# Performance work log

Measured on AMD Instinct MI355X. Metric: run time of the kernel, lower is better.

The kernel has to match this reference:

```python
import jax, jax.numpy as jnp
import numpy as np

COS_EPS = 1e-6
LN_EPS = 1e-5

def _cosine_sim(a, b):
    # PyTorch F.cosine_similarity(dim=1, eps): dot / (max(||a||,eps)*max(||b||,eps))
    dot = jnp.sum(a * b, axis=1)
    na = jnp.maximum(jnp.linalg.norm(a, axis=1), COS_EPS)
    nb = jnp.maximum(jnp.linalg.norm(b, axis=1), COS_EPS)
    return dot / (na * nb)

def _layer_norm(x, gamma, beta):
    mu = jnp.mean(x, axis=-1, keepdims=True)
    var = jnp.mean(jnp.square(x - mu), axis=-1, keepdims=True)
    return (x - mu) * jax.lax.rsqrt(var + LN_EPS) * gamma + beta

def setup_inputs() -> dict:
    B, I, H = 8192, 1024, 1024
    key = jax.random.key(0)
    ks = jax.random.split(key, 10)
    s_in = 1.0 / np.sqrt(I + H)
    s_im = 1.0 / np.sqrt(I)
    return {
        "x": jax.random.normal(ks[0], (B, I), jnp.float32),
        "hx": jax.random.normal(ks[1], (B, H), jnp.float32),
        "cx": jax.random.normal(ks[2], (B, H), jnp.float32),
        # main gate linear: [I+H, 4H]
        "W": jax.random.uniform(ks[3], (I + H, 4 * H), jnp.float32, -s_in, s_in),
        "b": jax.random.uniform(ks[4], (4 * H,), jnp.float32, -s_in, s_in),
        # input_mapped: [I, H]
        "Wm": jax.random.uniform(ks[5], (I, H), jnp.float32, -s_im, s_im),
        "bm": jax.random.uniform(ks[6], (H,), jnp.float32, -s_im, s_im),
        # 4 LayerNorms (i, f, g, o)
        "gammas": 1.0 + 0.1 * jax.random.normal(ks[7], (4, H), jnp.float32),
        "betas": 0.1 * jax.random.normal(ks[8], (4, H), jnp.float32),
    }

def reference(x, hx, cx, W, b, Wm, bm, gammas, betas):
    H = hx.shape[1]
    # cosine attention gate between mapped input and hidden state
    input_mapped = x @ Wm + bm                                   # [B, H]
    attn = jax.nn.sigmoid(_cosine_sim(input_mapped, hx))[:, None]  # [B, 1]
    x_mod = x + attn * x
    gates = jnp.concatenate([x_mod, hx], axis=1) @ W + b         # [B, 4H]
    i_g, f_g, g_g, o_g = jnp.split(gates, 4, axis=1)
    i_g = jax.nn.sigmoid(_layer_norm(i_g, gammas[0], betas[0]))
    f_g = jax.nn.sigmoid(_layer_norm(f_g, gammas[1], betas[1]))
    g_g = jnp.tanh(_layer_norm(g_g, gammas[2], betas[2]))
    o_g = jax.nn.sigmoid(_layer_norm(o_g, gammas[3], betas[3]))
    cx_new = f_g * cx + i_g * g_g
    hx_new = o_g * jnp.tanh(cx_new)
    gate_co = jax.nn.sigmoid((_cosine_sim(hx_new, cx_new)[:, None] + 1.0) / 2.0)
    hx_modulated = hx_new + hx_new * gate_co
    return (hx_modulated, cx_new)
```

## Files before the change

kernel.cpp:

```cpp
#include <hip/hip_runtime.h>
#include <hip/hip_bf16.h>

#define DEV __device__ __forceinline__

typedef unsigned short u16;
typedef unsigned int u32;
typedef __attribute__((ext_vector_type(8))) short bf16x8;
typedef __attribute__((ext_vector_type(4))) float f32x4;

DEV float bf2f(u16 v) { u32 u = ((u32)v) << 16; return __builtin_bit_cast(float, u); }
DEV u16 f2bf(float f) {
    u32 u = __builtin_bit_cast(u32, f);
    u32 r = (u + 0x7fffu + ((u >> 16) & 1u)) >> 16;
    return (u16)r;
}
DEV float lo16(u32 u) { return __builtin_bit_cast(float, u << 16); }
DEV float hi16(u32 u) { return __builtin_bit_cast(float, u & 0xffff0000u); }
DEV float sigm(float x) { return 1.f / (1.f + __expf(-x)); }
DEV float clamp4(float v) { return fminf(fmaxf(v, -1e4f), 1e4f); }
DEV float loadf(const void* p, size_t i, int isf) {
    return isf ? clamp4(((const float*)p)[i]) : clamp4(bf2f(((const u16*)p)[i]));
}
DEV void load8(const void* p, size_t off, int isf, float* o) {
    if (isf) {
        const float* s = (const float*)p + off;
#pragma unroll
        for (int e = 0; e < 8; ++e) o[e] = clamp4(s[e]);
    } else {
        uint4 q = *(const uint4*)((const u16*)p + off);
        o[0] = clamp4(lo16(q.x)); o[1] = clamp4(hi16(q.x));
        o[2] = clamp4(lo16(q.y)); o[3] = clamp4(hi16(q.y));
        o[4] = clamp4(lo16(q.z)); o[5] = clamp4(hi16(q.z));
        o[6] = clamp4(lo16(q.w)); o[7] = clamp4(hi16(q.w));
    }
}
DEV uint4 pack8(const float* a) {
    uint4 q;
    q.x = (u32)f2bf(a[0]) | ((u32)f2bf(a[1]) << 16);
    q.y = (u32)f2bf(a[2]) | ((u32)f2bf(a[3]) << 16);
    q.z = (u32)f2bf(a[4]) | ((u32)f2bf(a[5]) << 16);
    q.w = (u32)f2bf(a[6]) | ((u32)f2bf(a[7]) << 16);
    return q;
}
DEV void store8(void* p, size_t off, int isf, const float* a) {
    if (isf) {
        float* d = (float*)p + off;
        *(float4*)(d) = (float4){a[0], a[1], a[2], a[3]};
        *(float4*)(d + 4) = (float4){a[4], a[5], a[6], a[7]};
    } else {
        *(uint4*)((u16*)p + off) = pack8(a);
    }
}

DEV void gload16(const void* g, void* l) {
    __builtin_amdgcn_global_load_lds(
        (const __attribute__((address_space(1))) void*)g,
        (__attribute__((address_space(3))) void*)l, 16, 0, 0);
}

DEV void phase_gate() {
    __builtin_amdgcn_s_barrier();
    asm volatile("s_waitcnt lgkmcnt(0)" ::: "memory");
    __builtin_amdgcn_sched_barrier(0);
    __builtin_amdgcn_s_setprio(1);
}
DEV void phase_close() {
    __builtin_amdgcn_s_setprio(0);
    __builtin_amdgcn_s_barrier();
}

__global__ void detect_dtype(const u32* __restrict__ xw, u32* __restrict__ flag) {
    const int lane = threadIdx.x & 63;
    int cnt = 0;
    for (int k = 0; k < 32; ++k) {
        u32 e = (xw[lane + 64 * k] >> 7) & 0xff;
        cnt += (e >= 118 && e <= 130) ? 1 : 0;
    }
#pragma unroll
    for (int off = 32; off > 0; off >>= 1) cnt += __shfl_xor(cnt, off, 64);
    if (lane == 0) *flag = (cnt > 1024) ? 0u : 1u;
}

__global__ __launch_bounds__(256) void cvt2_bf16(
    const void* __restrict__ sa, const void* __restrict__ sb,
    u16* __restrict__ da, u16* __restrict__ db, int n8each,
    const u32* __restrict__ flagp) {
    const int isf = (int)*flagp;
    if (!isf) return;
    int i = blockIdx.x * 256 + threadIdx.x;
    const void* s; u16* d; int j;
    if (i < n8each) { s = sa; d = da; j = i; }
    else            { s = sb; d = db; j = i - n8each; }
    size_t off = (size_t)j * 8;
    float a[8];
    load8(s, off, 1, a);
    *(uint4*)(d + off) = pack8(a);
}

__global__ __launch_bounds__(256) void tr_any(const void* __restrict__ src,
                                              u16* __restrict__ dst,
                                              int R, int C,
                                              const u32* __restrict__ flagp) {
    const int isf = (int)*flagp;
    __shared__ __align__(16) u16 t[32][33];
    int tx = threadIdx.x & 31, ty = threadIdx.x >> 5;
    int c0 = blockIdx.x * 32, r0 = blockIdx.y * 32;
#pragma unroll
    for (int i = 0; i < 32; i += 8)
        t[ty + i][tx] = f2bf(loadf(src, (size_t)(r0 + ty + i) * C + (c0 + tx), isf));
    __syncthreads();
#pragma unroll
    for (int i = 0; i < 32; i += 8)
        dst[(size_t)(c0 + ty + i) * R + (r0 + tx)] = t[tx][ty + i];
}

__global__ __launch_bounds__(512, 2) void gemm256(
    const u16* __restrict__ A0c, const void* __restrict__ A0r,
    const u16* __restrict__ A1c, const void* __restrict__ A1r, int K0,
    const u16* __restrict__ Bt, const void* __restrict__ bias,
    const u32* __restrict__ flagp,
    u16* __restrict__ Cout, int M, int N, int K) {
    const int isf = (int)*flagp;
    const u16* const A0 = isf ? A0c : (const u16*)A0r;
    const u16* const A1 = isf ? A1c : (const u16*)A1r;
    __shared__ __align__(16) u16 lds[65536];
    u16* const ldsA = lds;
    u16* const ldsB = lds + 32768;
    const int tid = threadIdx.x;
    const int wave = tid >> 6, lane = tid & 63;
    const int wm = wave >> 2, wn = wave & 3;

    int bx = blockIdx.x, by = blockIdx.y;
    {
        const int gx = gridDim.x;
        const int nwg = gx * gridDim.y;
        if ((nwg & 7) == 0) {
            int lid = by * gx + bx;
            int swz = (lid & 7) * (nwg >> 3) + (lid >> 3);
            bx = swz % gx; by = swz / gx;
        }
    }
    const int m0 = by * 256, n0 = bx * 256;
    const int NT = K >> 6;

    size_t qA[2][2], qB[2][2];
#pragma unroll
    for (int h = 0; h < 2; ++h)
#pragma unroll
        for (int c = 0; c < 2; ++c) {
            int p = h * 16384 + c * 8192 + wave * 1024 + lane * 16;
            int lg = p ^ (((p >> 9) & 1) << 5);
            int s = lg >> 10, lr = (lg >> 6) & 15;
            int k = ((s & 1) << 5) + ((lg & 63) >> 1);
            int m = ((s >> 3) & 1) * 128 + ((s >> 4) & 1) * 64 +
                    ((s >> 1) & 3) * 16 + lr;
            qA[h][c] = (size_t)(m0 + m) * (size_t)K0 + (size_t)k;
            int ns = ((s >> 2) & 3) * 64 + ((s >> 4) & 1) * 32 +
                     ((s >> 1) & 1) * 16 + lr;
            int gn = (ns & ~63) | ((ns & 15) * 4 + ((ns >> 4) & 3));
            qB[h][c] = (size_t)(n0 + gn) * (size_t)K + (size_t)k;
        }

    const int mrow = lane & 15;
    const int kfr = (lane >> 4) * 8;
    const int aSwz = (mrow * 32 + kfr) ^ ((mrow & 8) << 1);

    f32x4 acc[8][4];
#pragma unroll
    for (int i = 0; i < 8; ++i)
#pragma unroll
        for (int j = 0; j < 4; ++j) acc[i][j] = (f32x4){0.f, 0.f, 0.f, 0.f};

#define ASEG(kt, AS_, KK_) const u16* AS_; int KK_; \
    if ((kt) < K0) { AS_ = A0; KK_ = (kt); } else { AS_ = A1; KK_ = (kt) - K0; }

#define RD_A(dst, off16) { const u16* ab_ = &ldsA[off16]; \
    _Pragma("unroll") for (int mt2 = 0; mt2 < 4; ++mt2) \
    _Pragma("unroll") for (int ks = 0; ks < 2; ++ks) \
        dst[mt2][ks] = *(const bf16x8*)&ab_[(mt2 * 2 + ks) * 512 + aSwz]; }

#define RD_B(dst, off16) { const u16* bb_ = &ldsB[off16]; \
    _Pragma("unroll") for (int nt2 = 0; nt2 < 2; ++nt2) \
    _Pragma("unroll") for (int ks = 0; ks < 2; ++ks) \
        dst[nt2][ks] = *(const bf16x8*)&bb_[(nt2 * 2 + ks) * 512 + aSwz]; }

#define MFMA_Q(AF, BF, MO, NO) \
    _Pragma("unroll") for (int mt2 = 0; mt2 < 4; ++mt2) \
    _Pragma("unroll") for (int nt2 = 0; nt2 < 2; ++nt2) \
    _Pragma("unroll") for (int ks = 0; ks < 2; ++ks) \
        acc[(MO) + mt2][(NO) + nt2] = __builtin_amdgcn_mfma_f32_16x16x32_bf16( \
            AF[mt2][ks], BF[nt2][ks], acc[(MO) + mt2][(NO) + nt2], 0, 0, 0);

    {
        { ASEG(0, As_, kk_);
          gload16(As_ + qA[0][0] + kk_, ldsA + wave * 512);
          gload16(As_ + qA[0][1] + kk_, ldsA + 4096 + wave * 512); }
        gload16(Bt + qB[1][0], ldsB + 8192 + wave * 512);
        gload16(Bt + qB[1][1], ldsB + 8192 + 4096 + wave * 512);
        { ASEG(0, As_, kk_);
          gload16(As_ + qA[1][0] + kk_, ldsA + 8192 + wave * 512);
          gload16(As_ + qA[1][1] + kk_, ldsA + 8192 + 4096 + wave * 512); }
        gload16(Bt + qB[0][0], ldsB + wave * 512);
        gload16(Bt + qB[0][1], ldsB + 4096 + wave * 512);
        { ASEG(64, As_, kk_);
          gload16(As_ + qA[0][0] + kk_, ldsA + 16384 + wave * 512);
          gload16(As_ + qA[0][1] + kk_, ldsA + 16384 + 4096 + wave * 512); }
        gload16(Bt + qB[1][0] + 64, ldsB + 16384 + 8192 + wave * 512);
        gload16(Bt + qB[1][1] + 64, ldsB + 16384 + 8192 + 4096 + wave * 512);
        { ASEG(64, As_, kk_);
          gload16(As_ + qA[1][0] + kk_, ldsA + 16384 + 8192 + wave * 512);
          gload16(As_ + qA[1][1] + kk_, ldsA + 16384 + 8192 + 4096 + wave * 512); }
        asm volatile("s_waitcnt vmcnt(6)" ::: "memory");
        __builtin_amdgcn_s_barrier();
    }

    bf16x8 af0[4][2], af1[4][2], bfA[2][2], bfB[2][2];
    for (int t = 0; t < NT; t += 2) {
        const bool more = (t + 2) < NT;
        const int kt1 = (t + 1) << 6, kt2 = (t + 2) << 6, kt3 = (t + 3) << 6;

        RD_A(af0, (wm * 8) * 512);
        RD_B(bfA, (wn * 4) * 512);
        gload16(Bt + qB[0][0] + kt1, ldsB + 16384 + wave * 512);
        gload16(Bt + qB[0][1] + kt1, ldsB + 16384 + 4096 + wave * 512);
        phase_gate();
        MFMA_Q(af0, bfA, 0, 0);
        phase_close();

        RD_B(bfB, (16 + wn * 4) * 512);
        if (more) { ASEG(kt2, As_, kk_);
            gload16(As_ + qA[0][0] + kk_, ldsA + wave * 512);
            gload16(As_ + qA[0][1] + kk_, ldsA + 4096 + wave * 512); }
        phase_gate();
        MFMA_Q(af0, bfB, 0, 2);
        phase_close();

        RD_A(af1, (16 + wm * 8) * 512);
        if (more) {
            gload16(Bt + qB[1][0] + kt2, ldsB + 8192 + wave * 512);
            gload16(Bt + qB[1][1] + kt2, ldsB + 8192 + 4096 + wave * 512); }
        phase_gate();
        MFMA_Q(af1, bfB, 4, 2);
        phase_close();

        if (more) { ASEG(kt2, As_, kk_);
            gload16(As_ + qA[1][0] + kk_, ldsA + 8192 + wave * 512);
            gload16(As_ + qA[1][1] + kk_, ldsA + 8192 + 4096 + wave * 512); }
        phase_gate();
        MFMA_Q(af1, bfA, 4, 0);
        __builtin_amdgcn_s_setprio(0);
        if (more) asm volatile("s_waitcnt vmcnt(6)" ::: "memory");
        else      asm volatile("s_waitcnt vmcnt(0)" ::: "memory");
        __builtin_amdgcn_s_barrier();

        RD_A(af0, 16384 + (wm * 8) * 512);
        RD_B(bfA, 16384 + (wn * 4) * 512);
        if (more) {
            gload16(Bt + qB[0][0] + kt2, ldsB + wave * 512);
            gload16(Bt + qB[0][1] + kt2, ldsB + 4096 + wave * 512); }
        phase_gate();
        MFMA_Q(af0, bfA, 0, 0);
        phase_close();

        RD_B(bfB, 16384 + (16 + wn * 4) * 512);
        if (more) { ASEG(kt3, As_, kk_);
            gload16(As_ + qA[0][0] + kk_, ldsA + 16384 + wave * 512);
            gload16(As_ + qA[0][1] + kk_, ldsA + 16384 + 4096 + wave * 512); }
        phase_gate();
        MFMA_Q(af0, bfB, 0, 2);
        phase_close();

        RD_A(af1, 16384 + (16 + wm * 8) * 512);
        if (more) {
            gload16(Bt + qB[1][0] + kt3, ldsB + 16384 + 8192 + wave * 512);
            gload16(Bt + qB[1][1] + kt3, ldsB + 16384 + 8192 + 4096 + wave * 512); }
        phase_gate();
        MFMA_Q(af1, bfB, 4, 2);
        phase_close();

        if (more) { ASEG(kt3, As_, kk_);
            gload16(As_ + qA[1][0] + kk_, ldsA + 16384 + 8192 + wave * 512);
            gload16(As_ + qA[1][1] + kk_, ldsA + 16384 + 8192 + 4096 + wave * 512); }
        phase_gate();
        MFMA_Q(af1, bfA, 4, 0);
        __builtin_amdgcn_s_setprio(0);
        if (more) asm volatile("s_waitcnt vmcnt(6)" ::: "memory");
        else      asm volatile("s_waitcnt vmcnt(0)" ::: "memory");
        __builtin_amdgcn_s_barrier();
    }
#undef ASEG
#undef RD_A
#undef RD_B
#undef MFMA_Q

    const int q = lane >> 4;
    const int cbase = n0 + wn * 64 + mrow * 4;
    float bv[4];
#pragma unroll
    for (int tt = 0; tt < 4; ++tt) bv[tt] = loadf(bias, cbase + tt, isf);
#pragma unroll
    for (int mt = 0; mt < 8; ++mt) {
        int row0 = m0 + wm * 128 + mt * 16 + q * 4;
#pragma unroll
        for (int r = 0; r < 4; ++r) {
            uint2 pk;
            pk.x = (u32)f2bf(acc[mt][0][r] + bv[0]) |
                   ((u32)f2bf(acc[mt][1][r] + bv[1]) << 16);
            pk.y = (u32)f2bf(acc[mt][2][r] + bv[2]) |
                   ((u32)f2bf(acc[mt][3][r] + bv[3]) << 16);
            *(uint2*)(Cout + (size_t)(row0 + r) * N + cbase) = pk;
        }
    }
}

__global__ __launch_bounds__(256) void attn_xmod(
    const u16* __restrict__ im,
    const u16* __restrict__ hxc, const void* __restrict__ hxr,
    const u16* __restrict__ xc, const void* __restrict__ xr,
    const u32* __restrict__ flagp, u16* __restrict__ xmod) {
    const int isf = (int)*flagp;
    const u16* hx = isf ? hxc : (const u16*)hxr;
    const u16* x = isf ? xc : (const u16*)xr;
    const int lane = threadIdx.x & 63;
    const int row = blockIdx.x * 4 + (threadIdx.x >> 6);
    float dot = 0.f, na = 0.f, nb = 0.f;
#pragma unroll
    for (int j = 0; j < 2; ++j) {
        size_t off = (size_t)row * 1024 + lane * 8 + j * 512;
        float a[8], h[8];
        load8(im, off, 0, a);
        load8(hx, off, 0, h);
#pragma unroll
        for (int e = 0; e < 8; ++e) {
            dot += a[e] * h[e]; na += a[e] * a[e]; nb += h[e] * h[e];
        }
    }
#pragma unroll
    for (int off = 32; off > 0; off >>= 1) {
        dot += __shfl_xor(dot, off, 64);
        na += __shfl_xor(na, off, 64);
        nb += __shfl_xor(nb, off, 64);
    }
    float cs = dot / (fmaxf(sqrtf(na), 1e-6f) * fmaxf(sqrtf(nb), 1e-6f));
    float fac = 1.f + sigm(cs);
#pragma unroll
    for (int j = 0; j < 2; ++j) {
        size_t off = (size_t)row * 1024 + lane * 8 + j * 512;
        float a[8];
        load8(x, off, 0, a);
#pragma unroll
        for (int e = 0; e < 8; ++e) a[e] *= fac;
        *(uint4*)(xmod + off) = pack8(a);
    }
}

__global__ __launch_bounds__(256) void ln_lstm(
    const u16* __restrict__ gates, const void* __restrict__ cx,
    const void* __restrict__ gammas, const void* __restrict__ betas,
    const u32* __restrict__ flagp, void* __restrict__ out, int BH) {
    const int isf = (int)*flagp;
    const int lane = threadIdx.x & 63;
    const int row = blockIdx.x * 4 + (threadIdx.x >> 6);
    float v[4][16];
    float s[4] = {0.f, 0.f, 0.f, 0.f}, ss[4] = {0.f, 0.f, 0.f, 0.f};
#pragma unroll
    for (int c = 0; c < 4; ++c) {
#pragma unroll
        for (int j = 0; j < 2; ++j) {
            size_t off = (size_t)row * 4096 + c * 1024 + lane * 8 + j * 512;
            float* vp = &v[c][j * 8];
            load8(gates, off, 0, vp);
#pragma unroll
            for (int e = 0; e < 8; ++e) { s[c] += vp[e]; ss[c] += vp[e] * vp[e]; }
        }
    }
#pragma unroll
    for (int off = 32; off > 0; off >>= 1) {
#pragma unroll
        for (int c = 0; c < 4; ++c) {
            s[c] += __shfl_xor(s[c], off, 64);
            ss[c] += __shfl_xor(ss[c], off, 64);
        }
    }
    float mean[4], rstd[4];
#pragma unroll
    for (int c = 0; c < 4; ++c) {
        mean[c] = s[c] * (1.f / 1024.f);
        float var = ss[c] * (1.f / 1024.f) - mean[c] * mean[c];
        rstd[c] = rsqrtf(fmaxf(var, 0.f) + 1e-5f);
    }
#pragma unroll
    for (int c = 0; c < 4; ++c) {
#pragma unroll
        for (int j = 0; j < 2; ++j) {
            size_t off = (size_t)(c * 1024 + lane * 8 + j * 512);
            float g[8], bb[8];
            load8(gammas, off, isf, g);
            load8(betas, off, isf, bb);
            float* vp = &v[c][j * 8];
#pragma unroll
            for (int e = 0; e < 8; ++e) {
                float y = (vp[e] - mean[c]) * rstd[c] * g[e] + bb[e];
                vp[e] = (c == 2) ? tanhf(y) : sigm(y);
            }
        }
    }
    float hn[16], cn[16];
    float dot = 0.f, nh = 0.f, nc = 0.f;
#pragma unroll
    for (int j = 0; j < 2; ++j) {
        size_t off = (size_t)row * 1024 + lane * 8 + j * 512;
        float cv[8];
        load8(cx, off, isf, cv);
#pragma unroll
        for (int e = 0; e < 8; ++e) {
            int idx = j * 8 + e;
            float c_new = v[1][idx] * cv[e] + v[0][idx] * v[2][idx];
            float h_new = v[3][idx] * tanhf(c_new);
            cn[idx] = c_new; hn[idx] = h_new;
            dot += h_new * c_new; nh += h_new * h_new; nc += c_new * c_new;
        }
    }
#pragma unroll
    for (int off = 32; off > 0; off >>= 1) {
        dot += __shfl_xor(dot, off, 64);
        nh += __shfl_xor(nh, off, 64);
        nc += __shfl_xor(nc, off, 64);
    }
    float cs = dot / (fmaxf(sqrtf(nh), 1e-6f) * fmaxf(sqrtf(nc), 1e-6f));
    float fac = 1.f + sigm((cs + 1.f) * 0.5f);
#pragma unroll
    for (int j = 0; j < 2; ++j) {
        size_t off = (size_t)row * 1024 + lane * 8 + j * 512;
        float ho[8];
#pragma unroll
        for (int e = 0; e < 8; ++e) ho[e] = hn[j * 8 + e] * fac;
        store8(out, off, isf, ho);
        store8(out, (size_t)BH + off, isf, &cn[j * 8]);
    }
}

__global__ void diag_k(u32* __restrict__ out, int ws_ok, int sizes_ok) {
    const int lane = threadIdx.x & 63;
    int mrow = lane & 15, quad = lane >> 4;
    bf16x8 af, bfr;
#pragma unroll
    for (int j = 0; j < 8; ++j) {
        int k = quad * 8 + j;
        af[j] = (short)f2bf((float)(((mrow * 7 + k * 3) % 11) - 5));
        bfr[j] = (short)f2bf((float)(((mrow * 5 + k * 2) % 13) - 6));
    }
    f32x4 cacc = (f32x4){0.f, 0.f, 0.f, 0.f};
    cacc = __builtin_amdgcn_mfma_f32_16x16x32_bf16(af, bfr, cacc, 0, 0, 0);
    int bad = 0;
#pragma unroll
    for (int r = 0; r < 4; ++r) {
        int mr = quad * 4 + r;
        float expv = 0.f;
        for (int k = 0; k < 32; ++k)
            expv += (float)(((mr * 7 + k * 3) % 11) - 5) *
                    (float)(((mrow * 5 + k * 2) % 13) - 6);
        if (fabsf(cacc[r] - expv) > 0.5f) bad = 1;
    }
    int mfma_bad = (__ballot(bad) != 0ull) ? 1 : 0;
    if (lane == 0) {
        if (!sizes_ok)     out[0] = __builtin_bit_cast(u32, 65536.f);
        else if (!ws_ok)   out[0] = __builtin_bit_cast(u32, 131072.f);
        else if (mfma_bad) out[0] = __builtin_bit_cast(u32, 32768.f);
    }
}

extern "C" void kernel_launch(void* const* d_in, const int* in_sizes, int n_in,
                              void* d_out, int out_size, void* d_ws, size_t ws_size,
                              hipStream_t stream) {
    const void* x   = d_in[0];
    const void* hx  = d_in[1];
    const void* cx  = d_in[2];
    const void* W   = d_in[3];
    const void* b   = d_in[4];
    const void* Wm  = d_in[5];
    const void* bm  = d_in[6];
    const void* gam = d_in[7];
    const void* bet = d_in[8];

    const int B = 8192, I = 1024, H = 1024;
    const int K2 = I + H, N2 = 4 * H;
    const size_t MiB = 1048576ull;

    char* ws = (char*)d_ws;
    u16* x_c   = (u16*)ws;
    u16* hx_c  = (u16*)(ws + 16 * MiB);
    u16* Wt    = (u16*)(ws + 32 * MiB);
    u16* Wmt   = (u16*)(ws + 48 * MiB);
    u16* gates = (u16*)(ws + 50 * MiB);
    u32* flag  = (u32*)(ws + 114 * MiB);
    u16* xmod  = (u16*)d_out;
    u16* imb   = (u16*)d_out + 8388608ull;

    const int sizes_ok =
        n_in == 9 && out_size == 16777216 &&
        in_sizes[0] == 8388608 && in_sizes[1] == 8388608 && in_sizes[2] == 8388608 &&
        in_sizes[3] == 8388608 && in_sizes[4] == 4096 && in_sizes[5] == 1048576 &&
        in_sizes[6] == 1024 && in_sizes[7] == 4096 && in_sizes[8] == 4096;
    const int ws_ok = ws_size >= 115 * MiB;

    if (sizes_ok && ws_ok) {
        detect_dtype<<<1, 64, 0, stream>>>((const u32*)x, flag);
        cvt2_bf16<<<8192, 256, 0, stream>>>(x, hx, x_c, hx_c, 1048576, flag);
        tr_any<<<dim3(H / 32, I / 32), 256, 0, stream>>>(Wm, Wmt, I, H, flag);
        tr_any<<<dim3(N2 / 32, K2 / 32), 256, 0, stream>>>(W, Wt, K2, N2, flag);
        gemm256<<<dim3(H / 256, B / 256), 512, 0, stream>>>(
            x_c, x, x_c, x, I, Wmt, bm, flag, imb, B, H, I);
        attn_xmod<<<dim3(B / 4), 256, 0, stream>>>(imb, hx_c, hx, x_c, x, flag, xmod);
        gemm256<<<dim3(N2 / 256, B / 256), 512, 0, stream>>>(
            xmod, xmod, hx_c, hx, I, Wt, b, flag, gates, B, N2, K2);
        ln_lstm<<<dim3(B / 4), 256, 0, stream>>>(gates, cx, gam, bet, flag,
                                                 d_out, B * H);
    }
    diag_k<<<1, 64, 0, stream>>>((u32*)d_out, ws_ok, sizes_ok);
}
```

Baseline: 416.8 us.

## Fuse dtype detection, input conversion and weight transposes into one prep kernel

Replaces four preprocessing launches (dtype detect, x/hx bf16 conversion, and the two weight transposes) with a single `prep` kernel. The grid is partitioned by block index into conversion blocks and transpose-tile blocks. The transpose now does vectorized 4-element loads and packed 4-element stores, and the fp32 load path uses float4 reads. To avoid a separate launch, every block redoes the dtype-detection sample from `x`. That adds redundant, mostly L2-cached reads plus a barrier per block, traded against fewer launches, no inter-kernel gaps, and wider transpose memory accesses.

```diff
diff --git a/kernel.cpp b/kernel.cpp
--- a/kernel.cpp
+++ b/kernel.cpp
@@ -24,8 +24,11 @@
 DEV void load8(const void* p, size_t off, int isf, float* o) {
     if (isf) {
         const float* s = (const float*)p + off;
-#pragma unroll
-        for (int e = 0; e < 8; ++e) o[e] = clamp4(s[e]);
+        float4 qa = *(const float4*)s, qb = *(const float4*)(s + 4);
+        o[0] = clamp4(qa.x); o[1] = clamp4(qa.y);
+        o[2] = clamp4(qa.z); o[3] = clamp4(qa.w);
+        o[4] = clamp4(qb.x); o[5] = clamp4(qb.y);
+        o[6] = clamp4(qb.z); o[7] = clamp4(qb.w);
     } else {
         uint4 q = *(const uint4*)((const u16*)p + off);
         o[0] = clamp4(lo16(q.x)); o[1] = clamp4(hi16(q.x));
@@ -69,49 +72,74 @@
     __builtin_amdgcn_s_barrier();
 }
 
-__global__ void detect_dtype(const u32* __restrict__ xw, u32* __restrict__ flag) {
-    const int lane = threadIdx.x & 63;
-    int cnt = 0;
-    for (int k = 0; k < 32; ++k) {
-        u32 e = (xw[lane + 64 * k] >> 7) & 0xff;
-        cnt += (e >= 118 && e <= 130) ? 1 : 0;
-    }
-#pragma unroll
-    for (int off = 32; off > 0; off >>= 1) cnt += __shfl_xor(cnt, off, 64);
-    if (lane == 0) *flag = (cnt > 1024) ? 0u : 1u;
-}
-
-__global__ __launch_bounds__(256) void cvt2_bf16(
-    const void* __restrict__ sa, const void* __restrict__ sb,
-    u16* __restrict__ da, u16* __restrict__ db, int n8each,
-    const u32* __restrict__ flagp) {
-    const int isf = (int)*flagp;
-    if (!isf) return;
-    int i = blockIdx.x * 256 + threadIdx.x;
-    const void* s; u16* d; int j;
-    if (i < n8each) { s = sa; d = da; j = i; }
-    else            { s = sb; d = db; j = i - n8each; }
-    size_t off = (size_t)j * 8;
-    float a[8];
-    load8(s, off, 1, a);
-    *(uint4*)(d + off) = pack8(a);
-}
-
-__global__ __launch_bounds__(256) void tr_any(const void* __restrict__ src,
-                                              u16* __restrict__ dst,
-                                              int R, int C,
-                                              const u32* __restrict__ flagp) {
-    const int isf = (int)*flagp;
-    __shared__ __align__(16) u16 t[32][33];
-    int tx = threadIdx.x & 31, ty = threadIdx.x >> 5;
-    int c0 = blockIdx.x * 32, r0 = blockIdx.y * 32;
-#pragma unroll
-    for (int i = 0; i < 32; i += 8)
-        t[ty + i][tx] = f2bf(loadf(src, (size_t)(r0 + ty + i) * C + (c0 + tx), isf));
+DEV void tr_tile(const void* __restrict__ src, u16* __restrict__ dst,
+                 int R, int C, int bx, int by, int isf, int tid,
+                 u16* tile ) {
+    const int c0 = bx * 32, r0 = by * 32;
+    const int ty = tid >> 3, tc = (tid & 7) * 4;
+    float v[4];
+    if (isf) {
+        float4 q = *(const float4*)((const float*)src + (size_t)(r0 + ty) * C + c0 + tc);
+        v[0] = clamp4(q.x); v[1] = clamp4(q.y); v[2] = clamp4(q.z); v[3] = clamp4(q.w);
+    } else {
+        uint2 q = *(const uint2*)((const u16*)src + (size_t)(r0 + ty) * C + c0 + tc);
+        v[0] = clamp4(lo16(q.x)); v[1] = clamp4(hi16(q.x));
+        v[2] = clamp4(lo16(q.y)); v[3] = clamp4(hi16(q.y));
+    }
+    uint2 w;
+    w.x = (u32)f2bf(v[0]) | ((u32)f2bf(v[1]) << 16);
+    w.y = (u32)f2bf(v[2]) | ((u32)f2bf(v[3]) << 16);
+    *(uint2*)&tile[ty * 36 + tc] = w;
     __syncthreads();
-#pragma unroll
-    for (int i = 0; i < 32; i += 8)
-        dst[(size_t)(c0 + ty + i) * R + (r0 + tx)] = t[tx][ty + i];
+    const int c = tid >> 3, rr = (tid & 7) * 4;
+    uint2 pk;
+    pk.x = (u32)tile[(rr + 0) * 36 + c] | ((u32)tile[(rr + 1) * 36 + c] << 16);
+    pk.y = (u32)tile[(rr + 2) * 36 + c] | ((u32)tile[(rr + 3) * 36 + c] << 16);
+    *(uint2*)&dst[(size_t)(c0 + c) * R + r0 + rr] = pk;
+}
+
+__global__ __launch_bounds__(256) void prep(
+    const void* __restrict__ x, const void* __restrict__ hx,
+    const void* __restrict__ Wm, const void* __restrict__ W,
+    u16* __restrict__ x_c, u16* __restrict__ hx_c,
+    u16* __restrict__ Wmt, u16* __restrict__ Wt,
+    u32* __restrict__ flag) {
+    __shared__ __align__(8) u16 tile[32 * 36];
+    __shared__ int isf_s;
+    const int tid = threadIdx.x;
+    const int bid = blockIdx.x;
+    if (tid < 64) {
+        const u32* xw = (const u32*)x;
+        int cnt = 0;
+        for (int k = 0; k < 32; ++k) {
+            u32 e = (xw[tid + 64 * k] >> 7) & 0xff;
+            cnt += (e >= 118 && e <= 130) ? 1 : 0;
+        }
+#pragma unroll
+        for (int off = 32; off > 0; off >>= 1) cnt += __shfl_xor(cnt, off, 64);
+        if (tid == 0) {
+            isf_s = (cnt > 1024) ? 0 : 1;
+            if (bid == 0) *flag = (u32)isf_s;
+        }
+    }
+    __syncthreads();
+    const int isf = isf_s;
+    if (bid < 8192) {
+        if (!isf) return;
+        const void* s; u16* d; int i;
+        if (bid < 4096) { s = x;  d = x_c;  i = bid * 256 + tid; }
+        else            { s = hx; d = hx_c; i = (bid - 4096) * 256 + tid; }
+        size_t off = (size_t)i * 8;
+        float a[8];
+        load8(s, off, 1, a);
+        *(uint4*)(d + off) = pack8(a);
+    } else if (bid < 9216) {
+        int b2 = bid - 8192;
+        tr_tile(Wm, Wmt, 1024, 1024, b2 & 31, b2 >> 5, isf, tid, tile);
+    } else {
+        int b2 = bid - 9216;
+        tr_tile(W, Wt, 2048, 4096, b2 & 127, b2 >> 7, isf, tid, tile);
+    }
 }
 
 __global__ __launch_bounds__(512, 2) void gemm256(
@@ -505,10 +533,7 @@
     const int ws_ok = ws_size >= 115 * MiB;
 
     if (sizes_ok && ws_ok) {
-        detect_dtype<<<1, 64, 0, stream>>>((const u32*)x, flag);
-        cvt2_bf16<<<8192, 256, 0, stream>>>(x, hx, x_c, hx_c, 1048576, flag);
-        tr_any<<<dim3(H / 32, I / 32), 256, 0, stream>>>(Wm, Wmt, I, H, flag);
-        tr_any<<<dim3(N2 / 32, K2 / 32), 256, 0, stream>>>(W, Wt, K2, N2, flag);
+        prep<<<17408, 256, 0, stream>>>(x, hx, Wm, W, x_c, hx_c, Wmt, Wt, flag);
         gemm256<<<dim3(H / 256, B / 256), 512, 0, stream>>>(
             x_c, x, x_c, x, I, Wmt, bm, flag, imb, B, H, I);
         attn_xmod<<<dim3(B / 4), 256, 0, stream>>>(imb, hx_c, hx, x_c, x, flag, xmod);
```

Result: no change. 413.7 us (-0.7%).
